# Kernel tuning notes

Measured on AMD Instinct MI355X. Metric: run time of the kernel, lower is better.

Reference implementation:

```python
import jax, jax.numpy as jnp
import numpy as np

B, T, I, H, O = 256, 500, 256, 256, 128

def _unif(key, shape, fan):
    bound = 1.0 / np.sqrt(fan)
    return jax.random.uniform(key, shape, jnp.float32, -bound, bound)

def setup_inputs() -> dict:
    key = jax.random.key(0)
    ks = jax.random.split(key, 12)
    return {
        "x": jax.random.normal(ks[0], (B, T, I), jnp.float32),
        # layer 0 (input_dim -> hidden)
        "W_ih0": _unif(ks[1], (H, I), H),
        "W_hh0": _unif(ks[2], (H, H), H),
        "b_ih0": _unif(ks[3], (H,), H),
        "b_hh0": _unif(ks[4], (H,), H),
        # layer 1 (hidden -> hidden)
        "W_ih1": _unif(ks[5], (H, H), H),
        "W_hh1": _unif(ks[6], (H, H), H),
        "b_ih1": _unif(ks[7], (H,), H),
        "b_hh1": _unif(ks[8], (H,), H),
        # fc head
        "fc_W": _unif(ks[9], (O, H), H),
        "fc_b": _unif(ks[10], (O,), H),
    }

def _rnn_layer(x_btf, W_ih, W_hh, b_ih, b_hh):
    # Precompute input projection for all timesteps in one GEMM: [B,T,H]
    xp = jnp.einsum("bti,hi->bth", x_btf, W_ih) + b_ih
    xp = jnp.swapaxes(xp, 0, 1)  # [T,B,H] for scan over time
    h0 = jnp.zeros((xp.shape[1], W_hh.shape[0]), xp.dtype)

    def step(h, xt):
        h_new = jnp.tanh(xt + h @ W_hh.T + b_hh)
        return h_new, h_new

    _, hs = jax.lax.scan(step, h0, xp)  # hs: [T,B,H]
    return jnp.swapaxes(hs, 0, 1)       # [B,T,H]

def reference(x, W_ih0, W_hh0, b_ih0, b_hh0, W_ih1, W_hh1, b_ih1, b_hh1, fc_W, fc_b):
    h1 = _rnn_layer(x, W_ih0, W_hh0, b_ih0, b_hh0)
    h2 = _rnn_layer(h1, W_ih1, W_hh1, b_ih1, b_hh1)
    logits = jnp.einsum("bth,oh->bto", h2, fc_W) + fc_b
    return jax.nn.sigmoid(logits)
```

## Files before the change

kernel.cpp:

```cpp
#include <hip/hip_runtime.h>
#include <hip/hip_fp16.h>

typedef _Float16 half_t;
typedef _Float16 half2_t __attribute__((ext_vector_type(2)));
typedef _Float16 f16x8 __attribute__((ext_vector_type(8)));
typedef float f32x4 __attribute__((ext_vector_type(4)));
typedef unsigned int u32;

#define MROWS 128000
#define KDIM 256

__device__ __forceinline__ float fdot2u(u32 w, u32 h, float acc) {
    return __builtin_amdgcn_fdot2(__builtin_bit_cast(half2_t, w),
                                  __builtin_bit_cast(half2_t, h), acc, false);
}

__global__ __launch_bounds__(256) void prep_kernel(
    const float* __restrict__ Wih0, const float* __restrict__ Whh0,
    const float* __restrict__ bih0, const float* __restrict__ bhh0,
    const float* __restrict__ Wih1, const float* __restrict__ Whh1,
    const float* __restrict__ bih1, const float* __restrict__ bhh1,
    const float* __restrict__ fcW,  const float* __restrict__ fcb,
    half_t* __restrict__ Wh0, half_t* __restrict__ Wh1, half_t* __restrict__ fcWh,
    u32* __restrict__ Wt0, u32* __restrict__ Wt1,
    float* __restrict__ bias0, float* __restrict__ bias1, float* __restrict__ bias2)
{
    int e = blockIdx.x * 256 + threadIdx.x;
    Wh0[e] = (half_t)Wih0[e];
    Wh1[e] = (half_t)Wih1[e];
    if (e < 32768) {
        fcWh[e] = (half_t)fcW[e];
        int k2 = e >> 8, j = e & 255;
        { half2_t p; p.x = (half_t)Whh0[j*256 + 2*k2]; p.y = (half_t)Whh0[j*256 + 2*k2 + 1];
          Wt0[e] = __builtin_bit_cast(u32, p); }
        { half2_t p; p.x = (half_t)Whh1[j*256 + 2*k2]; p.y = (half_t)Whh1[j*256 + 2*k2 + 1];
          Wt1[e] = __builtin_bit_cast(u32, p); }
    }
    if (e < 256) { bias0[e] = bih0[e] + bhh0[e]; bias1[e] = bih1[e] + bhh1[e]; }
    if (e < 128) { bias2[e] = fcb[e]; }
}

template<typename AT, typename OT, int NT, bool SIG>
__global__ __launch_bounds__(512) void gemm_bt(
    const AT* __restrict__ A, const half_t* __restrict__ W,
    const float* __restrict__ bias, OT* __restrict__ C)
{
    constexpr int K = KDIM;
    __shared__ __align__(16) half_t As[128][72];
    __shared__ __align__(16) half_t Ws[NT][72];
    __shared__ float bs[NT];
    const int tid  = threadIdx.x;
    const int row0 = blockIdx.x * 128;
    if (tid < NT) bs[tid] = bias[tid];
    constexpr int NFRAG = NT / 64;
    f32x4 acc[4][NFRAG] = {};
    const int lane = tid & 63;
    const int wid  = tid >> 6;
    const int wr = wid >> 2, wc = wid & 3;

    for (int kt = 0; kt < 4; ++kt) {
        const int k0 = kt * 64;
        if constexpr (sizeof(AT) == 4) {
            #pragma unroll
            for (int p = 0; p < 4; ++p) {
                int idx = p * 512 + tid; int r = idx >> 4; int c4 = (idx & 15) * 4;
                const float4 v = *(const float4*)(A + (size_t)(row0 + r) * K + k0 + c4);
                half2_t h01; h01.x = (half_t)v.x; h01.y = (half_t)v.y;
                half2_t h23; h23.x = (half_t)v.z; h23.y = (half_t)v.w;
                *(half2_t*)&As[r][c4]     = h01;
                *(half2_t*)&As[r][c4 + 2] = h23;
            }
        } else {
            #pragma unroll
            for (int p = 0; p < 2; ++p) {
                int idx = p * 512 + tid; int r = idx >> 3; int c8 = (idx & 7) * 8;
                uint4 v = *(const uint4*)(A + (size_t)(row0 + r) * K + k0 + c8);
                *(uint4*)&As[r][c8] = v;
            }
        }
        #pragma unroll
        for (int p = 0; p < NT / 64; ++p) {
            int idx = p * 512 + tid; int r = idx >> 3; int c8 = (idx & 7) * 8;
            uint4 v = *(const uint4*)(W + (size_t)r * K + k0 + c8);
            *(uint4*)&Ws[r][c8] = v;
        }
        __syncthreads();
        #pragma unroll
        for (int kkh = 0; kkh < 2; ++kkh) {
            const int kk = kkh * 32 + ((lane >> 4) * 8);
            f16x8 af[4], bf[NFRAG];
            #pragma unroll
            for (int m = 0; m < 4; ++m)
                af[m] = *(const f16x8*)&As[wr * 64 + m * 16 + (lane & 15)][kk];
            #pragma unroll
            for (int n = 0; n < NFRAG; ++n)
                bf[n] = *(const f16x8*)&Ws[wc * (NT / 4) + n * 16 + (lane & 15)][kk];
            #pragma unroll
            for (int m = 0; m < 4; ++m)
                #pragma unroll
                for (int n = 0; n < NFRAG; ++n)
                    acc[m][n] = __builtin_amdgcn_mfma_f32_16x16x32_f16(af[m], bf[n], acc[m][n], 0, 0, 0);
        }
        __syncthreads();
    }
    #pragma unroll
    for (int m = 0; m < 4; ++m)
        #pragma unroll
        for (int n = 0; n < NFRAG; ++n)
            #pragma unroll
            for (int jj = 0; jj < 4; ++jj) {
                int rl = wr * 64 + m * 16 + ((lane >> 4) * 4) + jj;
                int cl = wc * (NT / 4) + n * 16 + (lane & 15);
                float v = acc[m][n][jj] + bs[cl];
                if constexpr (SIG) v = 1.0f / (1.0f + __expf(-v));
                C[(size_t)(row0 + rl) * NT + cl] = (OT)v;
            }
}

__global__ __launch_bounds__(256, 1) void rnn_scan(
    const u32* __restrict__ Wt2,
    const half_t* __restrict__ xp,
    half_t* __restrict__ hout)
{
    __shared__ __align__(16) half_t hist[20][256];
    __shared__ __align__(16) half_t xpl[20][256];
    const int b = blockIdx.x;
    const int j = threadIdx.x;
    u32 w[128];
    #pragma unroll
    for (int k2 = 0; k2 < 128; ++k2) w[k2] = Wt2[k2 * 256 + j];
    const size_t base = (size_t)b * 500 * 256;
    const uint2* xg = (const uint2*)(xp + base);
    uint2* hg = (uint2*)(hout + base);

    hist[19][j] = (half_t)0.f;
    uint2 xr[5];
    #pragma unroll
    for (int p = 0; p < 5; ++p) ((uint2*)&xpl[0][0])[p * 256 + j] = xg[p * 256 + j];
    #pragma unroll
    for (int p = 0; p < 5; ++p) xr[p] = xg[1280 + p * 256 + j];
    __syncthreads();

    for (int ch = 0; ch < 25; ++ch) {
        for (int tc = 0; tc < 20; ++tc) {
            const int prev = (tc == 0) ? 19 : tc - 1;
            const uint4* hrow = (const uint4*)&hist[prev][0];
            float a0 = (float)xpl[tc][j], a1 = 0.f, a2 = 0.f, a3 = 0.f;
            uint4 hb[8];
            #pragma unroll
            for (int i = 0; i < 8; ++i) hb[i] = hrow[i];
            #pragma unroll
            for (int g = 0; g < 32; ++g) {
                uint4 hv = hb[g & 7];
                if (g + 8 < 32) hb[g & 7] = hrow[g + 8];
                a0 = fdot2u(w[4 * g + 0], hv.x, a0);
                a1 = fdot2u(w[4 * g + 1], hv.y, a1);
                a2 = fdot2u(w[4 * g + 2], hv.z, a2);
                a3 = fdot2u(w[4 * g + 3], hv.w, a3);
            }
            float h = tanhf((a0 + a1) + (a2 + a3));
            hist[tc][j] = (half_t)h;
            __syncthreads();
        }
        #pragma unroll
        for (int p = 0; p < 5; ++p)
            hg[(size_t)ch * 1280 + p * 256 + j] = ((const uint2*)&hist[0][0])[p * 256 + j];
        if (ch + 1 < 25) {
            #pragma unroll
            for (int p = 0; p < 5; ++p) ((uint2*)&xpl[0][0])[p * 256 + j] = xr[p];
            if (ch + 2 < 25) {
                #pragma unroll
                for (int p = 0; p < 5; ++p) xr[p] = xg[(size_t)(ch + 2) * 1280 + p * 256 + j];
            }
            __syncthreads();
        }
    }
}

extern "C" void kernel_launch(void* const* d_in, const int* in_sizes, int n_in,
                              void* d_out, int out_size, void* d_ws, size_t ws_size,
                              hipStream_t stream) {
    const float* x    = (const float*)d_in[0];
    const float* Wih0 = (const float*)d_in[1];
    const float* Whh0 = (const float*)d_in[2];
    const float* bih0 = (const float*)d_in[3];
    const float* bhh0 = (const float*)d_in[4];
    const float* Wih1 = (const float*)d_in[5];
    const float* Whh1 = (const float*)d_in[6];
    const float* bih1 = (const float*)d_in[7];
    const float* bhh1 = (const float*)d_in[8];
    const float* fcW  = (const float*)d_in[9];
    const float* fcb  = (const float*)d_in[10];

    char* ws = (char*)d_ws;
    size_t off = 0;
    auto alloc = [&](size_t bytes) { void* p = ws + off; off += (bytes + 255) & ~(size_t)255; return p; };
    half_t* xp_buf = (half_t*)alloc((size_t)MROWS * 256 * 2);
    half_t* h_buf  = (half_t*)alloc((size_t)MROWS * 256 * 2);
    half_t* Wh0    = (half_t*)alloc(65536 * 2);
    half_t* Wh1    = (half_t*)alloc(65536 * 2);
    half_t* fcWh   = (half_t*)alloc(32768 * 2);
    u32*    Wt0    = (u32*)alloc(32768 * 4);
    u32*    Wt1    = (u32*)alloc(32768 * 4);
    float*  bias0  = (float*)alloc(256 * 4);
    float*  bias1  = (float*)alloc(256 * 4);
    float*  bias2  = (float*)alloc(128 * 4);

    prep_kernel<<<256, 256, 0, stream>>>(Wih0, Whh0, bih0, bhh0, Wih1, Whh1, bih1, bhh1,
                                         fcW, fcb, Wh0, Wh1, fcWh, Wt0, Wt1, bias0, bias1, bias2);
    gemm_bt<float, half_t, 256, false><<<1000, 512, 0, stream>>>(x, Wh0, bias0, xp_buf);
    rnn_scan<<<256, 256, 0, stream>>>(Wt0, xp_buf, h_buf);
    gemm_bt<half_t, half_t, 256, false><<<1000, 512, 0, stream>>>(h_buf, Wh1, bias1, xp_buf);
    rnn_scan<<<256, 256, 0, stream>>>(Wt1, xp_buf, h_buf);
    gemm_bt<half_t, float, 128, true><<<1000, 512, 0, stream>>>(h_buf, fcWh, bias2, (float*)d_out);
}
```

Before: 743.6 us.

## Rewrite recurrent scan as batched MFMA over 16 sequences per block

Replaces the per-sequence fdot2 recurrence (one block per batch element) with a kernel where each block processes 16 batch rows, computing h@W_hh^T with 16x16x32 MFMA instructions, with the weights held in registers as fragments. Input projections are streamed into swizzled, double-buffered LDS through global_load_lds, and tanh is replaced by an exp2/rcp approximation. The grid shrinks from 256 to 16 blocks, so far fewer CUs are used. That trades parallelism for matrix-core throughput, with one serial 500-step chain per block. It also uses a less accurate tanh.

```diff
diff --git a/kernel.cpp b/kernel.cpp
--- a/kernel.cpp
+++ b/kernel.cpp
@@ -9,11 +9,6 @@
 
 #define MROWS 128000
 #define KDIM 256
-
-__device__ __forceinline__ float fdot2u(u32 w, u32 h, float acc) {
-    return __builtin_amdgcn_fdot2(__builtin_bit_cast(half2_t, w),
-                                  __builtin_bit_cast(half2_t, h), acc, false);
-}
 
 __global__ __launch_bounds__(256) void prep_kernel(
     const float* __restrict__ Wih0, const float* __restrict__ Whh0,
@@ -22,20 +17,15 @@
     const float* __restrict__ bih1, const float* __restrict__ bhh1,
     const float* __restrict__ fcW,  const float* __restrict__ fcb,
     half_t* __restrict__ Wh0, half_t* __restrict__ Wh1, half_t* __restrict__ fcWh,
-    u32* __restrict__ Wt0, u32* __restrict__ Wt1,
+    half_t* __restrict__ Whh0h, half_t* __restrict__ Whh1h,
     float* __restrict__ bias0, float* __restrict__ bias1, float* __restrict__ bias2)
 {
     int e = blockIdx.x * 256 + threadIdx.x;
     Wh0[e] = (half_t)Wih0[e];
     Wh1[e] = (half_t)Wih1[e];
-    if (e < 32768) {
-        fcWh[e] = (half_t)fcW[e];
-        int k2 = e >> 8, j = e & 255;
-        { half2_t p; p.x = (half_t)Whh0[j*256 + 2*k2]; p.y = (half_t)Whh0[j*256 + 2*k2 + 1];
-          Wt0[e] = __builtin_bit_cast(u32, p); }
-        { half2_t p; p.x = (half_t)Whh1[j*256 + 2*k2]; p.y = (half_t)Whh1[j*256 + 2*k2 + 1];
-          Wt1[e] = __builtin_bit_cast(u32, p); }
-    }
+    Whh0h[e] = (half_t)Whh0[e];
+    Whh1h[e] = (half_t)Whh1[e];
+    if (e < 32768) fcWh[e] = (half_t)fcW[e];
     if (e < 256) { bias0[e] = bih0[e] + bhh0[e]; bias1[e] = bih1[e] + bhh1[e]; }
     if (e < 128) { bias2[e] = fcb[e]; }
 }
@@ -117,63 +107,101 @@
             }
 }
 
-__global__ __launch_bounds__(256, 1) void rnn_scan(
-    const u32* __restrict__ Wt2,
+
+typedef __attribute__((address_space(1))) const unsigned gu32;
+typedef __attribute__((address_space(3))) unsigned lu32;
+
+__device__ __forceinline__ void stage16(const void* g, void* l) {
+    __builtin_amdgcn_global_load_lds((gu32*)g, (lu32*)l, 16, 0, 0);
+}
+
+__device__ __forceinline__ int swz(int b, int byteoff) {
+    return b * 512 + (byteoff ^ ((b & 7) << 4));
+}
+
+__device__ __forceinline__ float tanh_fast(float x) {
+    float e = __builtin_amdgcn_exp2f(x * 2.885390082f);
+    return __builtin_fmaf(-2.0f, __builtin_amdgcn_rcpf(e + 1.0f), 1.0f);
+}
+
+__global__ __launch_bounds__(256, 1) void rnn_scan_mfma(
+    const half_t* __restrict__ Whh,
     const half_t* __restrict__ xp,
     half_t* __restrict__ hout)
 {
-    __shared__ __align__(16) half_t hist[20][256];
-    __shared__ __align__(16) half_t xpl[20][256];
-    const int b = blockIdx.x;
-    const int j = threadIdx.x;
-    u32 w[128];
+    __shared__ __align__(16) char lds[32768];
+    char* const hs0 = lds;
+    char* const xs0 = lds + 16384;
+
+    const int tid = threadIdx.x;
+    const int w = tid >> 6, l = tid & 63, lq = l >> 4, bl = l & 15;
+    const int blk = blockIdx.x;
+
+    f16x8 wf[4][8];
     #pragma unroll
-    for (int k2 = 0; k2 < 128; ++k2) w[k2] = Wt2[k2 * 256 + j];
-    const size_t base = (size_t)b * 500 * 256;
-    const uint2* xg = (const uint2*)(xp + base);
-    uint2* hg = (uint2*)(hout + base);
-
-    hist[19][j] = (half_t)0.f;
-    uint2 xr[5];
-    #pragma unroll
-    for (int p = 0; p < 5; ++p) ((uint2*)&xpl[0][0])[p * 256 + j] = xg[p * 256 + j];
-    #pragma unroll
-    for (int p = 0; p < 5; ++p) xr[p] = xg[1280 + p * 256 + j];
+    for (int m = 0; m < 4; ++m)
+        #pragma unroll
+        for (int kt = 0; kt < 8; ++kt)
+            wf[m][kt] = *(const f16x8*)(Whh + (size_t)(w * 64 + m * 16 + bl) * 256 + kt * 32 + lq * 8);
+
+    uint4 z = {0u, 0u, 0u, 0u};
+    ((uint4*)hs0)[tid] = z;
+    ((uint4*)hs0)[256 + tid] = z;
+
+    const char* srcA; const char* srcB;
+    {
+        int b0 = tid >> 5,          c0 = (tid & 31) * 16;
+        int b1 = (256 + tid) >> 5,  c1 = (tid & 31) * 16;
+        srcA = (const char*)xp + (size_t)(blk * 16 + b0) * 500 * 512 + (c0 ^ ((b0 & 7) << 4));
+        srcB = (const char*)xp + (size_t)(blk * 16 + b1) * 500 * 512 + (c1 ^ ((b1 & 7) << 4));
+    }
+    stage16(srcA, xs0 + w * 1024);
+    stage16(srcB, xs0 + 4096 + w * 1024);
+
+    char* hst = (char*)hout + ((size_t)(blk * 16 + bl) * 500 * 256 + w * 64 + lq * 4) * 2;
+
     __syncthreads();
 
-    for (int ch = 0; ch < 25; ++ch) {
-        for (int tc = 0; tc < 20; ++tc) {
-            const int prev = (tc == 0) ? 19 : tc - 1;
-            const uint4* hrow = (const uint4*)&hist[prev][0];
-            float a0 = (float)xpl[tc][j], a1 = 0.f, a2 = 0.f, a3 = 0.f;
-            uint4 hb[8];
-            #pragma unroll
-            for (int i = 0; i < 8; ++i) hb[i] = hrow[i];
-            #pragma unroll
-            for (int g = 0; g < 32; ++g) {
-                uint4 hv = hb[g & 7];
-                if (g + 8 < 32) hb[g & 7] = hrow[g + 8];
-                a0 = fdot2u(w[4 * g + 0], hv.x, a0);
-                a1 = fdot2u(w[4 * g + 1], hv.y, a1);
-                a2 = fdot2u(w[4 * g + 2], hv.z, a2);
-                a3 = fdot2u(w[4 * g + 3], hv.w, a3);
-            }
-            float h = tanhf((a0 + a1) + (a2 + a3));
-            hist[tc][j] = (half_t)h;
-            __syncthreads();
-        }
-        #pragma unroll
-        for (int p = 0; p < 5; ++p)
-            hg[(size_t)ch * 1280 + p * 256 + j] = ((const uint2*)&hist[0][0])[p * 256 + j];
-        if (ch + 1 < 25) {
-            #pragma unroll
-            for (int p = 0; p < 5; ++p) ((uint2*)&xpl[0][0])[p * 256 + j] = xr[p];
-            if (ch + 2 < 25) {
-                #pragma unroll
-                for (int p = 0; p < 5; ++p) xr[p] = xg[(size_t)(ch + 2) * 1280 + p * 256 + j];
-            }
-            __syncthreads();
-        }
+    auto step = [&](int t, char* hcur, char* hnxt, const char* xcur, char* xnxt, bool last) {
+        srcA += 512; srcB += 512;
+        if (!last) {
+            stage16(srcA, xnxt + w * 1024);
+            stage16(srcB, xnxt + 4096 + w * 1024);
+        }
+        f16x8 bf[8];
+        #pragma unroll
+        for (int kt = 0; kt < 8; ++kt)
+            bf[kt] = *(const f16x8*)(hcur + swz(bl, kt * 64 + lq * 16));
+        f32x4 acc[4] = {};
+        #pragma unroll
+        for (int kt = 0; kt < 8; ++kt)
+            #pragma unroll
+            for (int m = 0; m < 4; ++m)
+                acc[m] = __builtin_amdgcn_mfma_f32_16x16x32_f16(wf[m][kt], bf[kt], acc[m], 0, 0, 0);
+        asm volatile("s_waitcnt vmcnt(2)" ::: "memory");
+        __builtin_amdgcn_sched_barrier(0);
+        #pragma unroll
+        for (int m = 0; m < 4; ++m) {
+            const int off = w * 128 + m * 32 + lq * 8;
+            uint2 xv = *(const uint2*)(xcur + swz(bl, off));
+            const half_t* xh = (const half_t*)&xv;
+            float v0 = tanh_fast(acc[m][0] + (float)xh[0]);
+            float v1 = tanh_fast(acc[m][1] + (float)xh[1]);
+            float v2 = tanh_fast(acc[m][2] + (float)xh[2]);
+            float v3 = tanh_fast(acc[m][3] + (float)xh[3]);
+            uint2 hv;
+            hv.x = __builtin_bit_cast(u32, __builtin_amdgcn_cvt_pkrtz(v0, v1));
+            hv.y = __builtin_bit_cast(u32, __builtin_amdgcn_cvt_pkrtz(v2, v3));
+            *(uint2*)(hnxt + swz(bl, off)) = hv;
+            *(uint2*)(hst + m * 32) = hv;
+        }
+        hst += 512;
+        __syncthreads();
+    };
+
+    for (int t2 = 0; t2 < 250; ++t2) {
+        step(2 * t2,     hs0,        hs0 + 8192, xs0,        xs0 + 8192, false);
+        step(2 * t2 + 1, hs0 + 8192, hs0,        xs0 + 8192, xs0,        2 * t2 + 1 == 499);
     }
 }
 
@@ -200,17 +228,18 @@
     half_t* Wh0    = (half_t*)alloc(65536 * 2);
     half_t* Wh1    = (half_t*)alloc(65536 * 2);
     half_t* fcWh   = (half_t*)alloc(32768 * 2);
-    u32*    Wt0    = (u32*)alloc(32768 * 4);
-    u32*    Wt1    = (u32*)alloc(32768 * 4);
+    half_t* Whh0h  = (half_t*)alloc(65536 * 2);
+    half_t* Whh1h  = (half_t*)alloc(65536 * 2);
     float*  bias0  = (float*)alloc(256 * 4);
     float*  bias1  = (float*)alloc(256 * 4);
     float*  bias2  = (float*)alloc(128 * 4);
 
     prep_kernel<<<256, 256, 0, stream>>>(Wih0, Whh0, bih0, bhh0, Wih1, Whh1, bih1, bhh1,
-                                         fcW, fcb, Wh0, Wh1, fcWh, Wt0, Wt1, bias0, bias1, bias2);
+                                         fcW, fcb, Wh0, Wh1, fcWh, Whh0h, Whh1h,
+                                         bias0, bias1, bias2);
     gemm_bt<float, half_t, 256, false><<<1000, 512, 0, stream>>>(x, Wh0, bias0, xp_buf);
-    rnn_scan<<<256, 256, 0, stream>>>(Wt0, xp_buf, h_buf);
+    rnn_scan_mfma<<<16, 256, 0, stream>>>(Whh0h, xp_buf, h_buf);
     gemm_bt<half_t, half_t, 256, false><<<1000, 512, 0, stream>>>(h_buf, Wh1, bias1, xp_buf);
-    rnn_scan<<<256, 256, 0, stream>>>(Wt1, xp_buf, h_buf);
+    rnn_scan_mfma<<<16, 256, 0, stream>>>(Whh1h, xp_buf, h_buf);
     gemm_bt<half_t, float, 128, true><<<1000, 512, 0, stream>>>(h_buf, fcWh, bias2, (float*)d_out);
 }
```

Result: slower. 1.282 ms (+72.4%).
